# Performance work log

Hardware: AMD Instinct MI355X
Metric: run time of the kernel (lower is better)

The kernel has to match this reference:

```python
import jax, jax.numpy as jnp
import numpy as np

EMBED_DIM = 1024
NUM_HEADS = 16
HEAD_DIM = EMBED_DIM // NUM_HEADS


def setup_inputs() -> dict:
    key = jax.random.key(0)
    ks = jax.random.split(key, 5)
    B, N, C = 4, 2048, EMBED_DIM
    x = jax.random.normal(ks[0], (B, N, C), dtype=jnp.float32)
    # Linear params (PyTorch layout: weight [out, in])
    s = 1.0 / np.sqrt(C)
    W_qkv = jax.random.uniform(ks[1], (3 * C, C), dtype=jnp.float32, minval=-s, maxval=s)
    b_qkv = jax.random.uniform(ks[2], (3 * C,), dtype=jnp.float32, minval=-s, maxval=s)
    W_out = jax.random.uniform(ks[3], (C, C), dtype=jnp.float32, minval=-s, maxval=s)
    b_out = jax.random.uniform(ks[4], (C,), dtype=jnp.float32, minval=-s, maxval=s)
    return {"x": x, "W_qkv": W_qkv, "b_qkv": b_qkv, "W_out": W_out, "b_out": b_out}


def _rotate_half(t):
    t1, t2 = jnp.split(t, 2, axis=-1)
    return jnp.concatenate((-t2, t1), axis=-1)


def _rope_cos_sin(seq_len, dim, dtype):
    inv_freq = 1.0 / (10000.0 ** (jnp.arange(0, dim, 2, dtype=jnp.float32) / dim))
    t = jnp.arange(seq_len, dtype=jnp.float32)
    freqs = jnp.einsum("i,j->ij", t, inv_freq)  # [N, dim/2]
    emb = jnp.concatenate((freqs, freqs), axis=-1)  # [N, dim]
    return emb.astype(dtype)


def reference(x, W_qkv, b_qkv, W_out, b_out):
    B, N, C = x.shape
    H, D = NUM_HEADS, HEAD_DIM
    qkv = x @ W_qkv.T + b_qkv  # [B, N, 3C]
    qkv = qkv.reshape(B, N, 3, H, D).transpose(2, 0, 3, 1, 4)  # [3, B, H, N, D]
    q, k, v = qkv[0], qkv[1], qkv[2]
    emb = _rope_cos_sin(N, D, x.dtype)
    cos = jnp.cos(emb)[None, None, :, :]  # [1,1,N,D]
    sin = jnp.sin(emb)[None, None, :, :]
    q = q * cos + _rotate_half(q) * sin
    k = k * cos + _rotate_half(k) * sin
    scale = D ** -0.5
    attn = jnp.einsum("bhnd,bhmd->bhnm", q, k) * scale  # [B,H,N,N]
    attn = jax.nn.softmax(attn, axis=-1)
    out = jnp.einsum("bhnm,bhmd->bhnd", attn, v)  # [B,H,N,D]
    out = out.transpose(0, 2, 1, 3).reshape(B, N, C)
    return out @ W_out.T + b_out
```

## Files before the change

kernel.cpp:

```cpp
#include <hip/hip_runtime.h>
#include <hip/hip_bf16.h>
#include <cstdint>
#include <cstddef>

#define SEQ 2048
#define NBATCH 4
#define EMB 1024
#define NH 16
#define HD 64
#define MTOT (NBATCH * SEQ)

typedef __attribute__((ext_vector_type(8))) short bf16x8;
typedef __attribute__((ext_vector_type(4))) float f32x4;
typedef __attribute__((ext_vector_type(16))) float f32x16;
typedef unsigned short u16;
typedef unsigned int u32;

__device__ __forceinline__ float bf2f(u16 v) {
  union { u32 u; float f; } c; c.u = ((u32)v) << 16; return c.f;
}
__device__ __forceinline__ u16 f2bf(float f) {
  union { float f; u32 u; } c; c.f = f;
  u32 u = c.u;
  return (u16)((u + 0x7FFFu + ((u >> 16) & 1u)) >> 16);
}
__device__ __forceinline__ u32 f2u(float f) {
  union { float f; u32 u; } c; c.f = f; return c.u;
}

__global__ void prep_kernel(const float* __restrict__ x, const float* __restrict__ wqkv,
                            const float* __restrict__ wout,
                            u16* __restrict__ xb, u16* __restrict__ wqkvb,
                            u16* __restrict__ woutb, float* __restrict__ tab2) {
  int tid = blockIdx.x * blockDim.x + threadIdx.x;
  int stride = gridDim.x * blockDim.x;
  for (int i = tid; i < MTOT * EMB / 4; i += stride) {
    float4 v = reinterpret_cast<const float4*>(x)[i];
    ushort4 o;
    o.x = f2bf(v.x); o.y = f2bf(v.y); o.z = f2bf(v.z); o.w = f2bf(v.w);
    reinterpret_cast<ushort4*>(xb)[i] = o;
  }
  for (int i = tid; i < 3 * EMB * EMB / 4; i += stride) {
    float4 v = reinterpret_cast<const float4*>(wqkv)[i];
    ushort4 o;
    o.x = f2bf(v.x); o.y = f2bf(v.y); o.z = f2bf(v.z); o.w = f2bf(v.w);
    reinterpret_cast<ushort4*>(wqkvb)[i] = o;
  }
  for (int i = tid; i < EMB * EMB / 4; i += stride) {
    float4 v = reinterpret_cast<const float4*>(wout)[i];
    ushort4 o;
    o.x = f2bf(v.x); o.y = f2bf(v.y); o.z = f2bf(v.z); o.w = f2bf(v.w);
    reinterpret_cast<ushort4*>(woutb)[i] = o;
  }
  for (int i = tid; i < SEQ * 32; i += stride) {
    int n = i >> 5, j = i & 31;
    float invf = 1.0f / powf(10000.0f, (float)(2 * j) / 64.0f);
    float ang = (float)n * invf;
    tab2[2 * i] = cosf(ang);
    tab2[2 * i + 1] = sinf(ang);
  }
}

__device__ __forceinline__ void gld_lds16(const u16* g, u16* l) {
  __builtin_amdgcn_global_load_lds((const __attribute__((address_space(1))) void*)g,
                                   (__attribute__((address_space(3))) void*)l, 16, 0, 0);
}

__global__ __launch_bounds__(256, 2)
void gemm_bt_f32(const u16* __restrict__ A, const u16* __restrict__ Bw,
                 const float* __restrict__ bias, float* __restrict__ Cout,
                 int N, int tiles_n) {
  __shared__ u16 lA[128 * 64];
  __shared__ u16 lB[128 * 64];
  const int K = 1024;
  int bm = blockIdx.x / tiles_n;
  int bn = blockIdx.x % tiles_n;
  int t = threadIdx.x;
  int wave = t >> 6, lane = t & 63;
  int wm = wave >> 1, wn = wave & 1;
  int l15 = lane & 15, l4 = lane >> 4;

  f32x4 acc[4][4];
#pragma unroll
  for (int i = 0; i < 4; ++i)
#pragma unroll
    for (int j = 0; j < 4; ++j) acc[i][j] = (f32x4){0.f, 0.f, 0.f, 0.f};

  int su[4], sr[4], sc[4];
#pragma unroll
  for (int i = 0; i < 4; ++i) {
    int u = (i * 4 + wave) * 64 + lane;
    su[i] = u;
    sr[i] = u >> 3;
    sc[i] = (u & 7) ^ (sr[i] & 7);
  }

  for (int kt = 0; kt < K / 64; ++kt) {
    if (kt) __syncthreads();
#pragma unroll
    for (int i = 0; i < 4; ++i) {
      gld_lds16(A + (size_t)(bm * 128 + sr[i]) * K + kt * 64 + sc[i] * 8, &lA[su[i] * 8]);
      gld_lds16(Bw + (size_t)(bn * 128 + sr[i]) * K + kt * 64 + sc[i] * 8, &lB[su[i] * 8]);
    }
    __syncthreads();
#pragma unroll
    for (int ks = 0; ks < 2; ++ks) {
      bf16x8 af[4], bfr[4];
#pragma unroll
      for (int mb = 0; mb < 4; ++mb) {
        int r = wm * 64 + mb * 16 + l15;
        int cc = (ks * 4 + l4) ^ (r & 7);
        af[mb] = *reinterpret_cast<const bf16x8*>(&lA[r * 64 + cc * 8]);
      }
#pragma unroll
      for (int nb = 0; nb < 4; ++nb) {
        int r = wn * 64 + nb * 16 + l15;
        int cc = (ks * 4 + l4) ^ (r & 7);
        bfr[nb] = *reinterpret_cast<const bf16x8*>(&lB[r * 64 + cc * 8]);
      }
#pragma unroll
      for (int mb = 0; mb < 4; ++mb)
#pragma unroll
        for (int nb = 0; nb < 4; ++nb)
          acc[mb][nb] = __builtin_amdgcn_mfma_f32_16x16x32_bf16(af[mb], bfr[nb], acc[mb][nb], 0, 0, 0);
    }
  }

#pragma unroll
  for (int mb = 0; mb < 4; ++mb)
#pragma unroll
    for (int nb = 0; nb < 4; ++nb) {
      int row0 = bm * 128 + wm * 64 + mb * 16 + l4 * 4;
      int col = bn * 128 + wn * 64 + nb * 16 + l15;
      float bv = bias[col];
#pragma unroll
      for (int r = 0; r < 4; ++r)
        Cout[(size_t)(row0 + r) * N + col] = acc[mb][nb][r] + bv;
    }
}

__global__ __launch_bounds__(256, 2)
void gemm_qkv_rope(const u16* __restrict__ A, const u16* __restrict__ Bw,
                   const float* __restrict__ bias, const float* __restrict__ tab2,
                   u16* __restrict__ Qb, u16* __restrict__ Kb, u16* __restrict__ Vtb) {
  __shared__ u16 lA[128 * 64];
  __shared__ u16 lB[128 * 64];
  const int K = 1024, tiles_n = 24;
  int bm = blockIdx.x / tiles_n;
  int bn = blockIdx.x % tiles_n;
  int t = threadIdx.x;
  int wave = t >> 6, lane = t & 63;
  int wm = wave >> 1, wn = wave & 1;
  int l15 = lane & 15, l4 = lane >> 4;

  f32x4 acc[4][4];
#pragma unroll
  for (int i = 0; i < 4; ++i)
#pragma unroll
    for (int j = 0; j < 4; ++j) acc[i][j] = (f32x4){0.f, 0.f, 0.f, 0.f};

  int su[4], sr[4], sc[4];
#pragma unroll
  for (int i = 0; i < 4; ++i) {
    int u = (i * 4 + wave) * 64 + lane;
    su[i] = u;
    sr[i] = u >> 3;
    sc[i] = (u & 7) ^ (sr[i] & 7);
  }
  int tauB[4];
#pragma unroll
  for (int i = 0; i < 4; ++i) {
    int rr = sr[i] & 63;
    tauB[i] = (sr[i] & 64) | (rr & 32) | ((rr & 15) << 1) | ((rr >> 4) & 1);
  }

  for (int kt = 0; kt < K / 64; ++kt) {
    if (kt) __syncthreads();
#pragma unroll
    for (int i = 0; i < 4; ++i) {
      gld_lds16(A + (size_t)(bm * 128 + sr[i]) * K + kt * 64 + sc[i] * 8, &lA[su[i] * 8]);
      gld_lds16(Bw + (size_t)(bn * 128 + tauB[i]) * K + kt * 64 + sc[i] * 8, &lB[su[i] * 8]);
    }
    __syncthreads();
#pragma unroll
    for (int ks = 0; ks < 2; ++ks) {
      bf16x8 af[4], bfr[4];
#pragma unroll
      for (int mb = 0; mb < 4; ++mb) {
        int r = wm * 64 + mb * 16 + l15;
        int cc = (ks * 4 + l4) ^ (r & 7);
        af[mb] = *reinterpret_cast<const bf16x8*>(&lA[r * 64 + cc * 8]);
      }
#pragma unroll
      for (int nb = 0; nb < 4; ++nb) {
        int r = wn * 64 + nb * 16 + l15;
        int cc = (ks * 4 + l4) ^ (r & 7);
        bfr[nb] = *reinterpret_cast<const bf16x8*>(&lB[r * 64 + cc * 8]);
      }
#pragma unroll
      for (int mb = 0; mb < 4; ++mb)
#pragma unroll
        for (int nb = 0; nb < 4; ++nb)
          acc[mb][nb] = __builtin_amdgcn_mfma_f32_16x16x32_bf16(af[mb], bfr[nb], acc[mb][nb], 0, 0, 0);
    }
  }

  int type = bn >> 3;
  int h = (bn * 2 + wn) & 15;
  int colbase = bn * 128 + wn * 64;
  float bv[4];
#pragma unroll
  for (int nb = 0; nb < 4; ++nb)
    bv[nb] = bias[colbase + 32 * (nb >> 1) + 2 * l15 + (nb & 1)];

  if (type < 2) {
    u16* dst0 = (type == 0) ? Qb : Kb;
    float qs = (type == 0) ? 0.1803368801111163f : 1.0f;
#pragma unroll
    for (int mb = 0; mb < 4; ++mb) {
      int row0 = bm * 128 + wm * 64 + mb * 16 + l4 * 4;
#pragma unroll
      for (int r = 0; r < 4; ++r) {
        int row = row0 + r;
        int bb = row >> 11, nl = row & 2047;
        float4 cs4 = *reinterpret_cast<const float4*>(tab2 + (size_t)nl * 64 + 4 * l15);
        float a0 = acc[mb][0][r] + bv[0];
        float a1 = acc[mb][1][r] + bv[1];
        float a2 = acc[mb][2][r] + bv[2];
        float a3 = acc[mb][3][r] + bv[3];
        float o0 = (a0 * cs4.x - a2 * cs4.y) * qs;
        float o2 = (a2 * cs4.x + a0 * cs4.y) * qs;
        float o1 = (a1 * cs4.z - a3 * cs4.w) * qs;
        float o3 = (a3 * cs4.z + a1 * cs4.w) * qs;
        u16* dst = dst0 + ((size_t)(bb * 16 + h) * SEQ + nl) * 64;
        u32 lo = (u32)f2bf(o0) | ((u32)f2bf(o1) << 16);
        u32 hi2 = (u32)f2bf(o2) | ((u32)f2bf(o3) << 16);
        *reinterpret_cast<u32*>(&dst[2 * l15]) = lo;
        *reinterpret_cast<u32*>(&dst[32 + 2 * l15]) = hi2;
      }
    }
  } else {
#pragma unroll
    for (int mb = 0; mb < 4; ++mb) {
      int row0 = bm * 128 + wm * 64 + mb * 16 + l4 * 4;
      int bb = row0 >> 11, nl0 = row0 & 2047;
#pragma unroll
      for (int nb = 0; nb < 4; ++nb) {
        int d = 32 * (nb >> 1) + 2 * l15 + (nb & 1);
        ushort4 pk;
        pk.x = f2bf(acc[mb][nb][0] + bv[nb]);
        pk.y = f2bf(acc[mb][nb][1] + bv[nb]);
        pk.z = f2bf(acc[mb][nb][2] + bv[nb]);
        pk.w = f2bf(acc[mb][nb][3] + bv[nb]);
        *reinterpret_cast<ushort4*>(&Vtb[((size_t)(bb * 16 + h) * 64 + d) * SEQ + nl0]) = pk;
      }
    }
  }
}

__global__ __launch_bounds__(256, 4)
void attn_kernel(const u16* __restrict__ Q, const u16* __restrict__ Kk,
                 const u16* __restrict__ Vt, u16* __restrict__ Out) {
  int bid = blockIdx.x;
  int swz = (bid & 7) * 128 + (bid >> 3);
  int bh = swz >> 4;
  int qt = swz & 15;
  int b = bh >> 4, h = bh & 15;
  int t = threadIdx.x;
  int wave = t >> 6, lane = t & 63;
  int l31 = lane & 31, hi = lane >> 5;

  __shared__ u16 lK[2][520 * 8];
  __shared__ u16 lV[2][520 * 8];

  const u16* Qh = Q + (size_t)bh * SEQ * 64;
  const u16* Kh = Kk + (size_t)bh * SEQ * 64;
  const u16* Vh = Vt + (size_t)bh * 64 * SEQ;
  int q0w = qt * 128 + wave * 32;

  bf16x8 qf[4];
#pragma unroll
  for (int dc = 0; dc < 4; ++dc)
    qf[dc] = *reinterpret_cast<const bf16x8*>(
        &Qh[(size_t)(q0w + l31) * 64 + dc * 16 + hi * 8]);

  f32x16 oacc[2];
#pragma unroll
  for (int db = 0; db < 2; ++db)
#pragma unroll
    for (int r = 0; r < 16; ++r) oacc[db][r] = 0.f;
  float dn = 0.f;

  bf16x8 kreg[2], vreg[2];
  auto stage_load = [&](int kt) {
#pragma unroll
    for (int p = 0; p < 2; ++p) {
      int u = p * 256 + t;
      int r = u >> 3, c = u & 7;
      kreg[p] = *reinterpret_cast<const bf16x8*>(&Kh[(size_t)(kt * 64 + r) * 64 + c * 8]);
      vreg[p] = *reinterpret_cast<const bf16x8*>(&Vh[(size_t)r * SEQ + kt * 64 + c * 8]);
    }
  };
  auto stage_write = [&](int buf) {
#pragma unroll
    for (int p = 0; p < 2; ++p) {
      int u = p * 256 + t;
      int r = u >> 3, c = u & 7;
      *reinterpret_cast<bf16x8*>(&lK[buf][(c * 65 + r) * 8]) = kreg[p];
      *reinterpret_cast<bf16x8*>(&lV[buf][(c * 65 + r) * 8]) = vreg[p];
    }
  };

  union PF { u32 w[4]; bf16x8 v; };
  int cur = 0;
  stage_load(0);
  stage_write(0);
  __syncthreads();
  for (int kt = 0; kt < SEQ / 64; ++kt) {
    if (kt + 1 < SEQ / 64) stage_load(kt + 1);

    f32x16 s[2];
#pragma unroll
    for (int cb = 0; cb < 2; ++cb)
#pragma unroll
      for (int r = 0; r < 16; ++r) s[cb][r] = 0.f;
    __builtin_amdgcn_s_setprio(1);
#pragma unroll
    for (int cb = 0; cb < 2; ++cb) {
#pragma unroll
      for (int dc = 0; dc < 4; ++dc) {
        bf16x8 kf = *reinterpret_cast<const bf16x8*>(
            &lK[cur][((dc * 2 + hi) * 65 + cb * 32 + l31) * 8]);
        s[cb] = __builtin_amdgcn_mfma_f32_32x32x16_bf16(kf, qf[dc], s[cb], 0, 0, 0);
      }
    }
    __builtin_amdgcn_s_setprio(0);

    PF pa[2][2];
#pragma unroll
    for (int cb = 0; cb < 2; ++cb) {
#pragma unroll
      for (int r = 0; r < 16; ++r) {
        float e = __builtin_amdgcn_exp2f(s[cb][r]);
        s[cb][r] = e;
        dn += e;
      }
#pragma unroll
      for (int c = 0; c < 2; ++c) {
        u32 u0 = f2u(s[cb][8 * c + 0]) + 0x8000u;
        u32 u1 = f2u(s[cb][8 * c + 1]) + 0x8000u;
        u32 u2 = f2u(s[cb][8 * c + 2]) + 0x8000u;
        u32 u3 = f2u(s[cb][8 * c + 3]) + 0x8000u;
        u32 u4 = f2u(s[cb][8 * c + 4]) + 0x8000u;
        u32 u5 = f2u(s[cb][8 * c + 5]) + 0x8000u;
        u32 u6 = f2u(s[cb][8 * c + 6]) + 0x8000u;
        u32 u7 = f2u(s[cb][8 * c + 7]) + 0x8000u;
        u32 a1 = __builtin_amdgcn_perm(u1, u0, 0x07060302);
        u32 a2 = __builtin_amdgcn_perm(u3, u2, 0x07060302);
        u32 b1 = __builtin_amdgcn_perm(u5, u4, 0x07060302);
        u32 b2 = __builtin_amdgcn_perm(u7, u6, 0x07060302);
        asm("v_permlane32_swap_b32 %0, %1" : "+v"(a1), "+v"(b1));
        asm("v_permlane32_swap_b32 %0, %1" : "+v"(a2), "+v"(b2));
        pa[cb][c].w[0] = a1; pa[cb][c].w[1] = a2;
        pa[cb][c].w[2] = b1; pa[cb][c].w[3] = b2;
      }
    }

    __builtin_amdgcn_s_setprio(1);
#pragma unroll
    for (int cb = 0; cb < 2; ++cb)
#pragma unroll
      for (int c = 0; c < 2; ++c)
#pragma unroll
        for (int db = 0; db < 2; ++db) {
          bf16x8 vf = *reinterpret_cast<const bf16x8*>(
              &lV[cur][((cb * 4 + c * 2 + hi) * 65 + db * 32 + l31) * 8]);
          oacc[db] = __builtin_amdgcn_mfma_f32_32x32x16_bf16(pa[cb][c].v, vf, oacc[db], 0, 0, 0);
        }
    __builtin_amdgcn_s_setprio(0);

    if (kt + 1 < SEQ / 64) stage_write(cur ^ 1);
    __syncthreads();
    cur ^= 1;
  }

  dn += __shfl_xor(dn, 32);
#pragma unroll
  for (int r = 0; r < 16; ++r) {
    int qrel = (r & 3) + 8 * (r >> 2) + 4 * hi;
    float dfull = __shfl(dn, qrel);
    float inv = __builtin_amdgcn_rcpf(dfull);
    int q = q0w + qrel;
#pragma unroll
    for (int db = 0; db < 2; ++db) {
      int d = db * 32 + l31;
      Out[(size_t)(b * SEQ + q) * EMB + h * 64 + d] = f2bf(oacc[db][r] * inv);
    }
  }
}

extern "C" void kernel_launch(void* const* d_in, const int* in_sizes, int n_in,
                              void* d_out, int out_size, void* d_ws, size_t ws_size,
                              hipStream_t stream) {
  const float* x = (const float*)d_in[0];
  const float* bqkv = (const float*)d_in[2];
  const float* bout = (const float*)d_in[4];
  float* out = (float*)d_out;

  char* ws = (char*)d_ws;
  size_t off = 0;
  auto alloc = [&](size_t bytes) {
    void* p = ws + off;
    off += (bytes + 255) & ~(size_t)255;
    return p;
  };
  u16* xb    = (u16*)alloc((size_t)MTOT * EMB * 2);
  u16* wqkvb = (u16*)alloc((size_t)3 * EMB * EMB * 2);
  u16* woutb = (u16*)alloc((size_t)EMB * EMB * 2);
  u16* Qb    = (u16*)alloc((size_t)64 * SEQ * HD * 2);
  u16* Kb    = (u16*)alloc((size_t)64 * SEQ * HD * 2);
  u16* Vtb   = (u16*)alloc((size_t)64 * HD * SEQ * 2);
  u16* aout  = (u16*)alloc((size_t)MTOT * EMB * 2);
  float* tab2 = (float*)alloc((size_t)SEQ * 32 * 2 * 4);
  (void)ws_size; (void)in_sizes; (void)n_in; (void)out_size;

  prep_kernel<<<2048, 256, 0, stream>>>(x, (const float*)d_in[1], (const float*)d_in[3],
                                        xb, wqkvb, woutb, tab2);
  gemm_qkv_rope<<<64 * 24, 256, 0, stream>>>(xb, wqkvb, bqkv, tab2, Qb, Kb, Vtb);
  attn_kernel<<<64 * 16, 256, 0, stream>>>(Qb, Kb, Vtb, aout);
  gemm_bt_f32<<<64 * 8, 256, 0, stream>>>(aout, woutb, bout, out, EMB, 8);
}
```

Baseline: 180.3 us.

## Pipeline QKV GEMM with triple-buffered LDS and 256x128 tiles

The QKV+RoPE GEMM now uses 512-thread blocks computing 256x128 tiles, so each B tile is shared by twice as many rows. LDS is triple-buffered, with global-to-LDS prefetch issued two k-steps ahead and explicit vmcnt waits, plus a single barrier per iteration. It also adds a block-index swizzle for L2 locality and raises MFMA issue priority with s_setprio. The aim is to hide global load latency and reduce barrier stalls, at the cost of 144KB of LDS per block, which limits occupancy.

```diff
diff --git a/kernel.cpp b/kernel.cpp
--- a/kernel.cpp
+++ b/kernel.cpp
@@ -139,15 +139,17 @@
     }
 }
 
-__global__ __launch_bounds__(256, 2)
+__global__ __launch_bounds__(512, 2)
 void gemm_qkv_rope(const u16* __restrict__ A, const u16* __restrict__ Bw,
                    const float* __restrict__ bias, const float* __restrict__ tab2,
                    u16* __restrict__ Qb, u16* __restrict__ Kb, u16* __restrict__ Vtb) {
-  __shared__ u16 lA[128 * 64];
-  __shared__ u16 lB[128 * 64];
-  const int K = 1024, tiles_n = 24;
-  int bm = blockIdx.x / tiles_n;
-  int bn = blockIdx.x % tiles_n;
+  __shared__ u16 lA[3][256 * 64];
+  __shared__ u16 lB[3][128 * 64];
+  const int K = 1024;
+  int bid = blockIdx.x;
+  int swz = (bid & 7) * 96 + (bid >> 3);
+  int bm = swz / 24;
+  int bn = swz % 24;
   int t = threadIdx.x;
   int wave = t >> 6, lane = t & 63;
   int wm = wave >> 1, wn = wave & 1;
@@ -159,50 +161,76 @@
 #pragma unroll
     for (int j = 0; j < 4; ++j) acc[i][j] = (f32x4){0.f, 0.f, 0.f, 0.f};
 
-  int su[4], sr[4], sc[4];
-#pragma unroll
-  for (int i = 0; i < 4; ++i) {
-    int u = (i * 4 + wave) * 64 + lane;
-    su[i] = u;
-    sr[i] = u >> 3;
-    sc[i] = (u & 7) ^ (sr[i] & 7);
-  }
-  int tauB[4];
-#pragma unroll
-  for (int i = 0; i < 4; ++i) {
-    int rr = sr[i] & 63;
-    tauB[i] = (sr[i] & 64) | (rr & 32) | ((rr & 15) << 1) | ((rr >> 4) & 1);
-  }
-
-  for (int kt = 0; kt < K / 64; ++kt) {
-    if (kt) __syncthreads();
-#pragma unroll
-    for (int i = 0; i < 4; ++i) {
-      gld_lds16(A + (size_t)(bm * 128 + sr[i]) * K + kt * 64 + sc[i] * 8, &lA[su[i] * 8]);
-      gld_lds16(Bw + (size_t)(bn * 128 + tauB[i]) * K + kt * 64 + sc[i] * 8, &lB[su[i] * 8]);
-    }
-    __syncthreads();
-#pragma unroll
-    for (int ks = 0; ks < 2; ++ks) {
-      bf16x8 af[4], bfr[4];
-#pragma unroll
-      for (int mb = 0; mb < 4; ++mb) {
+  size_t aoff[4]; int aldst[4];
+#pragma unroll
+  for (int j = 0; j < 4; ++j) {
+    int u = j * 512 + t;
+    int r = u >> 3, c = u & 7;
+    int sc = c ^ (r & 7);
+    aoff[j] = (size_t)(bm * 256 + r) * K + sc * 8;
+    aldst[j] = u * 8;
+  }
+  size_t boff[2]; int bldst[2];
+#pragma unroll
+  for (int j = 0; j < 2; ++j) {
+    int u = j * 512 + t;
+    int r = u >> 3, c = u & 7;
+    int sc = c ^ (r & 7);
+    int rr = r & 63;
+    int tr = (r & 64) | (rr & 32) | ((rr & 15) << 1) | ((rr >> 4) & 1);
+    boff[j] = (size_t)(bn * 128 + tr) * K + sc * 8;
+    bldst[j] = u * 8;
+  }
+  auto stage = [&](int buf, int kt) {
+    gld_lds16(Bw + boff[0] + kt * 64, &lB[buf][bldst[0]]);
+    gld_lds16(Bw + boff[1] + kt * 64, &lB[buf][bldst[1]]);
+    gld_lds16(A + aoff[0] + kt * 64, &lA[buf][aldst[0]]);
+    gld_lds16(A + aoff[1] + kt * 64, &lA[buf][aldst[1]]);
+    gld_lds16(A + aoff[2] + kt * 64, &lA[buf][aldst[2]]);
+    gld_lds16(A + aoff[3] + kt * 64, &lA[buf][aldst[3]]);
+  };
+
+  stage(0, 0);
+  stage(1, 1);
+  asm volatile("s_waitcnt vmcnt(6)" ::: "memory");
+  __builtin_amdgcn_s_barrier();
+
+  int cbuf = 0;
+  for (int kt = 0; kt < 16; ++kt) {
+    bf16x8 bfr[4][2];
+#pragma unroll
+    for (int nb = 0; nb < 4; ++nb)
+#pragma unroll
+      for (int kh = 0; kh < 2; ++kh) {
+        int r = wn * 64 + nb * 16 + l15;
+        int cc = (kh * 4 + l4) ^ (r & 7);
+        bfr[nb][kh] = *reinterpret_cast<const bf16x8*>(&lB[cbuf][r * 64 + cc * 8]);
+      }
+    int nbuf = cbuf + 2; if (nbuf >= 3) nbuf -= 3;
+    if (kt + 2 < 16) stage(nbuf, kt + 2);
+
+#pragma unroll
+    for (int mb = 0; mb < 4; ++mb) {
+      bf16x8 af[2];
+#pragma unroll
+      for (int kh = 0; kh < 2; ++kh) {
         int r = wm * 64 + mb * 16 + l15;
-        int cc = (ks * 4 + l4) ^ (r & 7);
-        af[mb] = *reinterpret_cast<const bf16x8*>(&lA[r * 64 + cc * 8]);
-      }
+        int cc = (kh * 4 + l4) ^ (r & 7);
+        af[kh] = *reinterpret_cast<const bf16x8*>(&lA[cbuf][r * 64 + cc * 8]);
+      }
+      __builtin_amdgcn_s_setprio(1);
 #pragma unroll
       for (int nb = 0; nb < 4; ++nb) {
-        int r = wn * 64 + nb * 16 + l15;
-        int cc = (ks * 4 + l4) ^ (r & 7);
-        bfr[nb] = *reinterpret_cast<const bf16x8*>(&lB[r * 64 + cc * 8]);
-      }
-#pragma unroll
-      for (int mb = 0; mb < 4; ++mb)
-#pragma unroll
-        for (int nb = 0; nb < 4; ++nb)
-          acc[mb][nb] = __builtin_amdgcn_mfma_f32_16x16x32_bf16(af[mb], bfr[nb], acc[mb][nb], 0, 0, 0);
-    }
+        acc[mb][nb] = __builtin_amdgcn_mfma_f32_16x16x32_bf16(af[0], bfr[nb][0], acc[mb][nb], 0, 0, 0);
+        acc[mb][nb] = __builtin_amdgcn_mfma_f32_16x16x32_bf16(af[1], bfr[nb][1], acc[mb][nb], 0, 0, 0);
+      }
+      __builtin_amdgcn_s_setprio(0);
+    }
+
+    if (kt < 14)       asm volatile("s_waitcnt vmcnt(6)" ::: "memory");
+    else if (kt == 14) asm volatile("s_waitcnt vmcnt(0)" ::: "memory");
+    if (kt < 15) __builtin_amdgcn_s_barrier();
+    cbuf = cbuf + 1; if (cbuf >= 3) cbuf -= 3;
   }
 
   int type = bn >> 3;
@@ -218,7 +246,7 @@
     float qs = (type == 0) ? 0.1803368801111163f : 1.0f;
 #pragma unroll
     for (int mb = 0; mb < 4; ++mb) {
-      int row0 = bm * 128 + wm * 64 + mb * 16 + l4 * 4;
+      int row0 = bm * 256 + wm * 64 + mb * 16 + l4 * 4;
 #pragma unroll
       for (int r = 0; r < 4; ++r) {
         int row = row0 + r;
@@ -242,7 +270,7 @@
   } else {
 #pragma unroll
     for (int mb = 0; mb < 4; ++mb) {
-      int row0 = bm * 128 + wm * 64 + mb * 16 + l4 * 4;
+      int row0 = bm * 256 + wm * 64 + mb * 16 + l4 * 4;
       int bb = row0 >> 11, nl0 = row0 & 2047;
 #pragma unroll
       for (int nb = 0; nb < 4; ++nb) {
@@ -426,7 +454,7 @@
 
   prep_kernel<<<2048, 256, 0, stream>>>(x, (const float*)d_in[1], (const float*)d_in[3],
                                         xb, wqkvb, woutb, tab2);
-  gemm_qkv_rope<<<64 * 24, 256, 0, stream>>>(xb, wqkvb, bqkv, tab2, Qb, Kb, Vtb);
+  gemm_qkv_rope<<<768, 512, 0, stream>>>(xb, wqkvb, bqkv, tab2, Qb, Kb, Vtb);
   attn_kernel<<<64 * 16, 256, 0, stream>>>(Qb, Kb, Vtb, aout);
   gemm_bt_f32<<<64 * 8, 256, 0, stream>>>(aout, woutb, bout, out, EMB, 8);
 }
```

New measurement: 201.8 us. 11.9% more time.
